# Optimization experiments

Measured on AMD Instinct MI355X. Metric: run time of the kernel, lower is better.

Reference implementation:

```python
import jax, jax.numpy as jnp
import numpy as np
from jax import lax

B, T, I, H = 4096, 512, 1, 32

def setup_inputs() -> dict:
    key = jax.random.key(0)
    ks = jax.random.split(key, 7)
    s = 1.0 / np.sqrt(H)
    return {
        "x": jax.random.normal(ks[0], (B, T, I), dtype=jnp.float32),
        "W_ih": jax.random.uniform(ks[1], (4 * H, I), minval=-s, maxval=s, dtype=jnp.float32),
        "W_hh": jax.random.uniform(ks[2], (4 * H, H), minval=-s, maxval=s, dtype=jnp.float32),
        "b_ih": jax.random.uniform(ks[3], (4 * H,), minval=-s, maxval=s, dtype=jnp.float32),
        "b_hh": jax.random.uniform(ks[4], (4 * H,), minval=-s, maxval=s, dtype=jnp.float32),
        "W_lin": jax.random.uniform(ks[5], (1, H), minval=-s, maxval=s, dtype=jnp.float32),
        "b_lin": jax.random.uniform(ks[6], (1,), minval=-s, maxval=s, dtype=jnp.float32),
    }

def reference(x, W_ih, W_hh, b_ih, b_hh, W_lin, b_lin):
    b, t, _ = x.shape
    h = W_hh.shape[1]
    # Precompute input contribution to all gates for all timesteps: [T,B,4H]
    xg = jnp.einsum('bti,gi->tbg', x, W_ih) + b_ih + b_hh

    def step(carry, xt):
        hs, cs = carry
        g = xt + hs @ W_hh.T  # [B,4H], PyTorch gate order i,f,g,o
        i = jax.nn.sigmoid(g[:, :h])
        f = jax.nn.sigmoid(g[:, h:2 * h])
        gg = jnp.tanh(g[:, 2 * h:3 * h])
        o = jax.nn.sigmoid(g[:, 3 * h:])
        cs = f * cs + i * gg
        hs = o * jnp.tanh(cs)
        return (hs, cs), None

    h0 = jnp.zeros((b, h), dtype=x.dtype)
    c0 = jnp.zeros((b, h), dtype=x.dtype)
    (h_last, _), _ = lax.scan(step, (h0, c0), xg)
    # final linear on last hidden state: [B,1]
    return h_last @ W_lin.T + b_lin
```

## Files before the change

kernel.cpp:

```cpp
#include <hip/hip_runtime.h>


typedef float f32x4 __attribute__((ext_vector_type(4)));
typedef short s16x8 __attribute__((ext_vector_type(8)));

#define L2E 1.44269504088896340736f
#define MFMA(a, b, c) __builtin_amdgcn_mfma_f32_16x16x32_bf16((a), (b), (c), 0, 0, 0)

__device__ __forceinline__ unsigned bfpack(float a, float b) {
    return __builtin_amdgcn_perm(__float_as_uint(b), __float_as_uint(a), 0x07060302u);
}
__device__ __forceinline__ float hi_f(float f) {
    return __uint_as_float(__float_as_uint(f) & 0xFFFF0000u);
}
__device__ __forceinline__ float sig_pre(float t) {
    return __builtin_amdgcn_rcpf(1.0f + __builtin_amdgcn_exp2f(t));
}
__device__ __forceinline__ float tanh_pre(float t) {
    return fmaf(__builtin_amdgcn_rcpf(1.0f + __builtin_amdgcn_exp2f(t)), 2.0f, -1.0f);
}

#define RSTR 40

__global__ __launch_bounds__(128, 2) void lstm_mfma_kernel(
    const float* __restrict__ x,
    const float* __restrict__ W_ih,
    const float* __restrict__ W_hh,
    const float* __restrict__ b_ih,
    const float* __restrict__ b_hh,
    const float* __restrict__ W_lin,
    const float* __restrict__ b_lin,
    float* __restrict__ out,
    int B)
{
    __shared__ unsigned short Hb[2][8][RSTR];
    __shared__ float plds[4][2];

    const int tid  = (int)threadIdx.x;
    const int w    = tid >> 6;
    const int lane = tid & 63;
    const int col  = lane & 15;
    const int g    = lane >> 4;

    for (int i = tid; i < 2 * 8 * RSTR; i += 128)
        ((unsigned short*)Hb)[i] = 0;

    const int m4   = col & 3;
    const int rrow = (m4 == 0) ? 2 * (col >> 2)
                   : (m4 == 1) ? 2 * (col >> 2) + 1
                   : (m4 - 2);
    const unsigned short* Ard0 = &Hb[0][rrow][8 * g];
    const unsigned short* Ard1 = &Hb[1][rrow][8 * g];

    unsigned short* Whi0 = &Hb[0][2 * g + 0][2 * col + w];
    unsigned short* Wlo0 = &Hb[0][2 * g + 1][2 * col + w];
    unsigned short* Whi1 = &Hb[1][2 * g + 0][2 * col + w];
    unsigned short* Wlo1 = &Hb[1][2 * g + 1][2 * col + w];

    s16x8 bhi[4], blo[4];
    float wihs[4];
    f32x4 biasC[4];
#pragma unroll
    for (int j = 0; j < 4; ++j) {
        const int t  = w + 2 * j;
        const int gr = t * 16 + col;
        const float sc = (j == 2) ? (-2.0f * L2E) : (-L2E);
        const float* wr = &W_hh[gr * 32];
        float4 wA = *reinterpret_cast<const float4*>(&wr[g * 4]);
        float4 wB = *reinterpret_cast<const float4*>(&wr[g * 4 + 16]);
        const float a0 = wA.x * sc, a1 = wA.y * sc, a2 = wA.z * sc, a3 = wA.w * sc;
        const float b0 = wB.x * sc, b1 = wB.y * sc, b2 = wB.z * sc, b3 = wB.w * sc;
        union { unsigned u[4]; s16x8 s; } H, L;
        H.u[0] = bfpack(a0, b0); H.u[1] = bfpack(a1, b1);
        H.u[2] = bfpack(a2, b2); H.u[3] = bfpack(a3, b3);
        L.u[0] = bfpack(a0 - hi_f(a0), b0 - hi_f(b0));
        L.u[1] = bfpack(a1 - hi_f(a1), b1 - hi_f(b1));
        L.u[2] = bfpack(a2 - hi_f(a2), b2 - hi_f(b2));
        L.u[3] = bfpack(a3 - hi_f(a3), b3 - hi_f(b3));
        bhi[j] = H.s; blo[j] = L.s;
        wihs[j] = W_ih[gr] * sc;
        const float bb = (b_ih[gr] + b_hh[gr]) * sc;
        biasC[j] = f32x4{bb, 0.0f, 0.0f, 0.0f};
    }

    const int b_glob = blockIdx.x * 4 + g;
    const int bc     = b_glob < B ? b_glob : (B - 1);
    const float* xb  = x + (size_t)bc * 512;

    float4 xA = *reinterpret_cast<const float4*>(xb);
    float4 xB = *reinterpret_cast<const float4*>(xb + 4);

    float cc = 0.0f, hh = 0.0f;
    __syncthreads();

    for (int tc = 0; tc < 64; ++tc) {
        const int nbase = ((tc + 1) & 63) * 8;
        const float4 nA = *reinterpret_cast<const float4*>(xb + nbase);
        const float4 nB = *reinterpret_cast<const float4*>(xb + nbase + 4);
        const float xts[8] = {xA.x, xA.y, xA.z, xA.w, xB.x, xB.y, xB.z, xB.w};

#pragma unroll
        for (int s = 0; s < 8; ++s) {
            const float xt = xts[s];

            const s16x8 af = *reinterpret_cast<const s16x8*>((s & 1) ? Ard1 : Ard0);

            f32x4 acc[4];
#pragma unroll
            for (int j = 0; j < 4; ++j) acc[j] = MFMA(af, bhi[j], biasC[j]);
#pragma unroll
            for (int j = 0; j < 4; ++j) acc[j] = MFMA(af, blo[j], acc[j]);

            float gt[4];
#pragma unroll
            for (int j = 0; j < 4; ++j)
                gt[j] = fmaf(xt, wihs[j], acc[j][0] + acc[j][1]);

            const float i_ = sig_pre(gt[0]);
            const float f_ = sig_pre(gt[1]);
            const float G_ = tanh_pre(gt[2]);
            const float o_ = sig_pre(gt[3]);

            cc = fmaf(f_, cc, i_ * G_);
            hh = o_ * tanh_pre(cc * (-2.0f * L2E));

            const unsigned uh = __float_as_uint(hh);
            const float lo = hh - __uint_as_float(uh & 0xFFFF0000u);
            *((s & 1) ? Whi0 : Whi1) = (unsigned short)(uh >> 16);
            *((s & 1) ? Wlo0 : Wlo1) = (unsigned short)(__float_as_uint(lo) >> 16);
            __syncthreads();
        }
        xA = nA; xB = nB;
    }

    float part = hh * W_lin[col + 16 * w];
    part += __shfl_xor(part, 1, 64);
    part += __shfl_xor(part, 2, 64);
    part += __shfl_xor(part, 4, 64);
    part += __shfl_xor(part, 8, 64);
    if (col == 0) plds[g][w] = part;
    __syncthreads();
    if (w == 0 && col == 0 && b_glob < B)
        out[b_glob] = plds[g][0] + plds[g][1] + b_lin[0];
}

extern "C" void kernel_launch(void* const* d_in, const int* in_sizes, int n_in,
                              void* d_out, int out_size, void* d_ws, size_t ws_size,
                              hipStream_t stream) {
    const float* x     = (const float*)d_in[0];
    const float* W_ih  = (const float*)d_in[1];
    const float* W_hh  = (const float*)d_in[2];
    const float* b_ih  = (const float*)d_in[3];
    const float* b_hh  = (const float*)d_in[4];
    const float* W_lin = (const float*)d_in[5];
    const float* b_lin = (const float*)d_in[6];
    float* out = (float*)d_out;

    const int B = in_sizes[0] / 512;
    const int blocks = (B + 3) / 4;

    lstm_mfma_kernel<<<blocks, 128, 0, stream>>>(x, W_ih, W_hh, b_ih, b_hh,
                                                 W_lin, b_lin, out, B);
}
```

Baseline: 145.1 us.

## Process two independent batch groups per block to interleave recurrent chains

Each block now carries two sets of four sequences, each with its own double-buffered hidden-state LDS and its own register state. The MFMA, activation and store work for the two sets is interleaved within each timestep, and the block count is halved. This is meant to hide MFMA and transcendental latency and to spread the per-step barrier cost over twice the work. In exchange, register pressure rises, launch bounds are relaxed, and there are fewer blocks in flight.

```diff
diff --git a/kernel.cpp b/kernel.cpp
--- a/kernel.cpp
+++ b/kernel.cpp
@@ -22,7 +22,7 @@
 
 #define RSTR 40
 
-__global__ __launch_bounds__(128, 2) void lstm_mfma_kernel(
+__global__ __launch_bounds__(128, 1) void lstm_mfma_kernel(
     const float* __restrict__ x,
     const float* __restrict__ W_ih,
     const float* __restrict__ W_hh,
@@ -33,8 +33,8 @@
     float* __restrict__ out,
     int B)
 {
-    __shared__ unsigned short Hb[2][8][RSTR];
-    __shared__ float plds[4][2];
+    __shared__ unsigned short Hb[2][2][8][RSTR];
+    __shared__ float plds[2][4][2];
 
     const int tid  = (int)threadIdx.x;
     const int w    = tid >> 6;
@@ -42,20 +42,26 @@
     const int col  = lane & 15;
     const int g    = lane >> 4;
 
-    for (int i = tid; i < 2 * 8 * RSTR; i += 128)
+    for (int i = tid; i < 2 * 2 * 8 * RSTR; i += 128)
         ((unsigned short*)Hb)[i] = 0;
 
     const int m4   = col & 3;
     const int rrow = (m4 == 0) ? 2 * (col >> 2)
                    : (m4 == 1) ? 2 * (col >> 2) + 1
                    : (m4 - 2);
-    const unsigned short* Ard0 = &Hb[0][rrow][8 * g];
-    const unsigned short* Ard1 = &Hb[1][rrow][8 * g];
+    const unsigned short* ArdP0 = &Hb[0][0][rrow][8 * g];
+    const unsigned short* ArdP1 = &Hb[0][1][rrow][8 * g];
+    const unsigned short* ArdQ0 = &Hb[1][0][rrow][8 * g];
+    const unsigned short* ArdQ1 = &Hb[1][1][rrow][8 * g];
 
-    unsigned short* Whi0 = &Hb[0][2 * g + 0][2 * col + w];
-    unsigned short* Wlo0 = &Hb[0][2 * g + 1][2 * col + w];
-    unsigned short* Whi1 = &Hb[1][2 * g + 0][2 * col + w];
-    unsigned short* Wlo1 = &Hb[1][2 * g + 1][2 * col + w];
+    unsigned short* WhiP0 = &Hb[0][0][2 * g + 0][2 * col + w];
+    unsigned short* WloP0 = &Hb[0][0][2 * g + 1][2 * col + w];
+    unsigned short* WhiP1 = &Hb[0][1][2 * g + 0][2 * col + w];
+    unsigned short* WloP1 = &Hb[0][1][2 * g + 1][2 * col + w];
+    unsigned short* WhiQ0 = &Hb[1][0][2 * g + 0][2 * col + w];
+    unsigned short* WloQ0 = &Hb[1][0][2 * g + 1][2 * col + w];
+    unsigned short* WhiQ1 = &Hb[1][1][2 * g + 0][2 * col + w];
+    unsigned short* WloQ1 = &Hb[1][1][2 * g + 1][2 * col + w];
 
     s16x8 bhi[4], blo[4];
     float wihs[4];
@@ -83,65 +89,87 @@
         biasC[j] = f32x4{bb, 0.0f, 0.0f, 0.0f};
     }
 
-    const int b_glob = blockIdx.x * 4 + g;
-    const int bc     = b_glob < B ? b_glob : (B - 1);
-    const float* xb  = x + (size_t)bc * 512;
+    const int bP = blockIdx.x * 8 + g;
+    const int bQ = bP + 4;
+    const int bPc = bP < B ? bP : (B - 1);
+    const int bQc = bQ < B ? bQ : (B - 1);
+    const float* xbP = x + (size_t)bPc * 512;
+    const float* xbQ = x + (size_t)bQc * 512;
 
-    float4 xA = *reinterpret_cast<const float4*>(xb);
-    float4 xB = *reinterpret_cast<const float4*>(xb + 4);
+    float4 xAP = *reinterpret_cast<const float4*>(xbP);
+    float4 xBP = *reinterpret_cast<const float4*>(xbP + 4);
+    float4 xAQ = *reinterpret_cast<const float4*>(xbQ);
+    float4 xBQ = *reinterpret_cast<const float4*>(xbQ + 4);
 
-    float cc = 0.0f, hh = 0.0f;
+    float cP = 0.0f, hP = 0.0f, cQ = 0.0f, hQ = 0.0f;
     __syncthreads();
 
     for (int tc = 0; tc < 64; ++tc) {
         const int nbase = ((tc + 1) & 63) * 8;
-        const float4 nA = *reinterpret_cast<const float4*>(xb + nbase);
-        const float4 nB = *reinterpret_cast<const float4*>(xb + nbase + 4);
-        const float xts[8] = {xA.x, xA.y, xA.z, xA.w, xB.x, xB.y, xB.z, xB.w};
+        const float4 nAP = *reinterpret_cast<const float4*>(xbP + nbase);
+        const float4 nBP = *reinterpret_cast<const float4*>(xbP + nbase + 4);
+        const float4 nAQ = *reinterpret_cast<const float4*>(xbQ + nbase);
+        const float4 nBQ = *reinterpret_cast<const float4*>(xbQ + nbase + 4);
+        const float xtsP[8] = {xAP.x, xAP.y, xAP.z, xAP.w, xBP.x, xBP.y, xBP.z, xBP.w};
+        const float xtsQ[8] = {xAQ.x, xAQ.y, xAQ.z, xAQ.w, xBQ.x, xBQ.y, xBQ.z, xBQ.w};
 
 #pragma unroll
         for (int s = 0; s < 8; ++s) {
-            const float xt = xts[s];
+            const s16x8 afP = *reinterpret_cast<const s16x8*>((s & 1) ? ArdP1 : ArdP0);
+            const s16x8 afQ = *reinterpret_cast<const s16x8*>((s & 1) ? ArdQ1 : ArdQ0);
 
-            const s16x8 af = *reinterpret_cast<const s16x8*>((s & 1) ? Ard1 : Ard0);
+            f32x4 aP[4], aQ[4];
+#pragma unroll
+            for (int j = 0; j < 4; ++j) aP[j] = MFMA(afP, bhi[j], biasC[j]);
+#pragma unroll
+            for (int j = 0; j < 4; ++j) aQ[j] = MFMA(afQ, bhi[j], biasC[j]);
+#pragma unroll
+            for (int j = 0; j < 4; ++j) aP[j] = MFMA(afP, blo[j], aP[j]);
+#pragma unroll
+            for (int j = 0; j < 4; ++j) aQ[j] = MFMA(afQ, blo[j], aQ[j]);
 
-            f32x4 acc[4];
+            float gP[4], gQ[4];
 #pragma unroll
-            for (int j = 0; j < 4; ++j) acc[j] = MFMA(af, bhi[j], biasC[j]);
+            for (int j = 0; j < 4; ++j) gP[j] = fmaf(xtsP[s], wihs[j], aP[j][0] + aP[j][1]);
 #pragma unroll
-            for (int j = 0; j < 4; ++j) acc[j] = MFMA(af, blo[j], acc[j]);
+            for (int j = 0; j < 4; ++j) gQ[j] = fmaf(xtsQ[s], wihs[j], aQ[j][0] + aQ[j][1]);
 
-            float gt[4];
-#pragma unroll
-            for (int j = 0; j < 4; ++j)
-                gt[j] = fmaf(xt, wihs[j], acc[j][0] + acc[j][1]);
+            const float iP = sig_pre(gP[0]),  iQ = sig_pre(gQ[0]);
+            const float fP = sig_pre(gP[1]),  fQ = sig_pre(gQ[1]);
+            const float GP = tanh_pre(gP[2]), GQ = tanh_pre(gQ[2]);
+            const float oP = sig_pre(gP[3]),  oQ = sig_pre(gQ[3]);
 
-            const float i_ = sig_pre(gt[0]);
-            const float f_ = sig_pre(gt[1]);
-            const float G_ = tanh_pre(gt[2]);
-            const float o_ = sig_pre(gt[3]);
+            cP = fmaf(fP, cP, iP * GP);
+            cQ = fmaf(fQ, cQ, iQ * GQ);
+            hP = oP * tanh_pre(cP * (-2.0f * L2E));
+            hQ = oQ * tanh_pre(cQ * (-2.0f * L2E));
 
-            cc = fmaf(f_, cc, i_ * G_);
-            hh = o_ * tanh_pre(cc * (-2.0f * L2E));
-
-            const unsigned uh = __float_as_uint(hh);
-            const float lo = hh - __uint_as_float(uh & 0xFFFF0000u);
-            *((s & 1) ? Whi0 : Whi1) = (unsigned short)(uh >> 16);
-            *((s & 1) ? Wlo0 : Wlo1) = (unsigned short)(__float_as_uint(lo) >> 16);
+            const unsigned uP = __float_as_uint(hP);
+            const float lP = hP - __uint_as_float(uP & 0xFFFF0000u);
+            const unsigned uQ = __float_as_uint(hQ);
+            const float lQ = hQ - __uint_as_float(uQ & 0xFFFF0000u);
+            *((s & 1) ? WhiP0 : WhiP1) = (unsigned short)(uP >> 16);
+            *((s & 1) ? WloP0 : WloP1) = (unsigned short)(__float_as_uint(lP) >> 16);
+            *((s & 1) ? WhiQ0 : WhiQ1) = (unsigned short)(uQ >> 16);
+            *((s & 1) ? WloQ0 : WloQ1) = (unsigned short)(__float_as_uint(lQ) >> 16);
             __syncthreads();
         }
-        xA = nA; xB = nB;
+        xAP = nAP; xBP = nBP; xAQ = nAQ; xBQ = nBQ;
     }
 
-    float part = hh * W_lin[col + 16 * w];
-    part += __shfl_xor(part, 1, 64);
-    part += __shfl_xor(part, 2, 64);
-    part += __shfl_xor(part, 4, 64);
-    part += __shfl_xor(part, 8, 64);
-    if (col == 0) plds[g][w] = part;
+    float pPv = hP * W_lin[col + 16 * w];
+    float pQv = hQ * W_lin[col + 16 * w];
+#pragma unroll
+    for (int off = 8; off; off >>= 1) {
+        pPv += __shfl_xor(pPv, off, 64);
+        pQv += __shfl_xor(pQv, off, 64);
+    }
+    if (col == 0) { plds[0][g][w] = pPv; plds[1][g][w] = pQv; }
     __syncthreads();
-    if (w == 0 && col == 0 && b_glob < B)
-        out[b_glob] = plds[g][0] + plds[g][1] + b_lin[0];
+    if (w == 0 && col == 0) {
+        if (bP < B) out[bP] = plds[0][g][0] + plds[0][g][1] + b_lin[0];
+        if (bQ < B) out[bQ] = plds[1][g][0] + plds[1][g][1] + b_lin[0];
+    }
 }
 
 extern "C" void kernel_launch(void* const* d_in, const int* in_sizes, int n_in,
@@ -157,7 +185,7 @@
     float* out = (float*)d_out;
 
     const int B = in_sizes[0] / 512;
-    const int blocks = (B + 3) / 4;
+    const int blocks = (B + 7) / 8;
 
     lstm_mfma_kernel<<<blocks, 128, 0, stream>>>(x, W_ih, W_hh, b_ih, b_hh,
                                                  W_lin, b_lin, out, B);
```

New measurement: 279.6 us. 1.93x slower.
